# Kernel optimization log

Measured on AMD Instinct MI355X. Metric: run time of the kernel, lower is better.

The kernel has to match this reference:

```python
import jax, jax.numpy as jnp
import numpy as np

TEMPERATURE = 0.04


def _d3tod2(t):
    # 'c h w -> (h w) c'
    c, h, w = t.shape
    return jnp.transpose(t, (1, 2, 0)).reshape(h * w, c)


def setup_inputs() -> dict:
    key = jax.random.key(0)
    k1, k2 = jax.random.split(key)
    B, C, H, W = 4, 128, 96, 96
    # scale 0.05 keeps dot/temperature in a numerically sane range for exp
    x = jax.random.normal(k1, (B, C, H, W), dtype=jnp.float32) * 0.05
    label = jax.random.randint(k2, (B, 1, H, W), 0, 3, dtype=jnp.int32)
    return {"x": x, "label": label}


def reference(x, label):
    B, C, H, W = x.shape
    hw = H * W
    feat_1 = _d3tod2(x[0])                     # [HW, C]
    feat_2 = _d3tod2(x[1])                     # [HW, C]
    gt1 = label[0, 0].reshape(hw)              # [HW]
    gt2 = label[1, 0].reshape(hw)              # [HW]
    sim = jnp.exp(jnp.matmul(feat_1, feat_2.T) / TEMPERATURE)  # [HW, HW]
    mask = gt1[:, None] == gt2[None, :]        # [HW, HW] label-equality
    pos_sum = jnp.sum(jnp.where(mask, sim, jnp.zeros((), sim.dtype)))
    total_sum = jnp.sum(sim)
    loss = -jnp.log(pos_sum / total_sum) / (hw * hw)
    return loss
```

## Files before the change

### kernel.cpp

```cpp
#include <hip/hip_runtime.h>
#include <hip/hip_bf16.h>

#define HW 9216
#define CDIM 128
#define BM 256
#define BN 64
#define JT 4
#define GRID_I (HW / BM)
#define GRID_J (HW / (BN * JT))
#define NPART (GRID_I * GRID_J)
#define LDP (CDIM + 8)

using bf16 = __hip_bfloat16;
typedef __attribute__((ext_vector_type(16))) float f32x16;
typedef __attribute__((ext_vector_type(8))) short s16x8;

#define EXP_SCALE 36.067376022224085f

#if __has_builtin(__builtin_amdgcn_exp2f)
#define FEXP2(x) __builtin_amdgcn_exp2f(x)
#else
#define FEXP2(x) exp2f(x)
#endif

__global__ __launch_bounds__(256) void prep_kernel(const float* __restrict__ x,
                                                   bf16* __restrict__ feat) {
    __shared__ float tile[64][65];
    const float* xs = x + (size_t)blockIdx.z * CDIM * HW;
    bf16* fs = feat + (size_t)blockIdx.z * HW * CDIM;
    float scale = (blockIdx.z == 0) ? EXP_SCALE : 1.0f;

    int p0 = blockIdx.x * 64;
    int c0 = blockIdx.y * 64;
    int t  = threadIdx.x;

    int pc = t & 63;
    int cr = t >> 6;
#pragma unroll
    for (int i = 0; i < 16; ++i) {
        int cl = cr + i * 4;
        tile[cl][pc] = xs[(size_t)(c0 + cl) * HW + p0 + pc];
    }
    __syncthreads();

    int cc = t & 63;
    int pr = t >> 6;
#pragma unroll
    for (int i = 0; i < 16; ++i) {
        int pl = pr + i * 4;
        fs[(size_t)(p0 + pl) * CDIM + c0 + cc] = __float2bfloat16(tile[cc][pl] * scale);
    }
}

__global__ __launch_bounds__(512, 4) void simsum_kernel(const bf16* __restrict__ feat1,
                                                        const bf16* __restrict__ feat2,
                                                        const int* __restrict__ label,
                                                        float* __restrict__ partials) {
    __shared__ bf16 Bs[2][BN][LDP];
    __shared__ float red[16];

    int t    = threadIdx.x;
    int w    = t >> 6;
    int lane = t & 63;
    int cl   = lane & 31;
    int hi   = lane >> 5;

    int i0  = blockIdx.x * BM;
    int jb  = blockIdx.y * (BN * JT);
    int r0w = i0 + w * 32;

    s16x8 af[8];
    {
        const bf16* arow = &feat1[(size_t)(r0w + cl) * CDIM + hi * 8];
#pragma unroll
        for (int s = 0; s < 8; ++s)
            af[s] = *(const s16x8*)(arow + s * 16);
    }

    int4 g1i[4];
#pragma unroll
    for (int q = 0; q < 4; ++q)
        g1i[q] = *(const int4*)(&label[r0w + 4 * hi + 8 * q]);

    int srow = t >> 4;
    int sch8 = (t & 15) * 8;
    s16x8 rb[2];

    auto load_tile = [&](int tt) {
        const bf16* base = &feat2[(size_t)(jb + tt * BN + srow) * CDIM + sch8];
        rb[0] = *(const s16x8*)(base);
        rb[1] = *(const s16x8*)(base + 32 * CDIM);
    };
    auto write_tile = [&](int b) {
        *(s16x8*)(&Bs[b][srow][sch8])      = rb[0];
        *(s16x8*)(&Bs[b][srow + 32][sch8]) = rb[1];
    };

    load_tile(0);  write_tile(0);
    load_tile(1);  write_tile(1);
    load_tile(2);
    asm volatile("s_waitcnt lgkmcnt(0)" ::: "memory");
    __builtin_amdgcn_sched_barrier(0);
    __builtin_amdgcn_s_barrier();

    const int* lab2 = label + HW;
    float tot0 = 0.f, tot1 = 0.f, pos0 = 0.f, pos1 = 0.f;

#pragma unroll
    for (int tt = 0; tt < JT; ++tt) {
        int g2a = lab2[jb + tt * BN + cl];
        int g2b = lab2[jb + tt * BN + 32 + cl];

        f32x16 acc0 = {}, acc1 = {};
#pragma unroll
        for (int s = 0; s < 8; ++s) {
            const bf16* bp = &Bs[tt & 1][cl][s * 16 + hi * 8];
            s16x8 b0 = *(const s16x8*)(bp);
            s16x8 b1 = *(const s16x8*)(bp + (size_t)32 * LDP);
            acc0 = __builtin_amdgcn_mfma_f32_32x32x16_bf16(af[s], b0, acc0, 0, 0, 0);
            acc1 = __builtin_amdgcn_mfma_f32_32x32x16_bf16(af[s], b1, acc1, 0, 0, 0);
        }

        __builtin_amdgcn_sched_barrier(0);
        __builtin_amdgcn_s_barrier();

        if (tt + 2 < JT) write_tile(tt & 1);
        if (tt + 3 < JT) load_tile(tt + 3);

#pragma unroll
        for (int r = 0; r < 16; ++r) {
            int g1 = ((const int*)g1i)[r];
            float e0 = FEXP2(acc0[r]);
            tot0 += e0;
            pos0 += (g1 == g2a) ? e0 : 0.f;
            float e1 = FEXP2(acc1[r]);
            tot1 += e1;
            pos1 += (g1 == g2b) ? e1 : 0.f;
        }

        if (tt + 1 < JT) {
            asm volatile("s_waitcnt lgkmcnt(0)" ::: "memory");
            __builtin_amdgcn_sched_barrier(0);
            __builtin_amdgcn_s_barrier();
        }
    }

    float tot = tot0 + tot1, pos = pos0 + pos1;
#pragma unroll
    for (int off = 32; off; off >>= 1) {
        tot += __shfl_down(tot, off);
        pos += __shfl_down(pos, off);
    }
    if (lane == 0) { red[w * 2] = tot; red[w * 2 + 1] = pos; }
    __syncthreads();
    if (t == 0) {
        float T = 0.f, P = 0.f;
#pragma unroll
        for (int q = 0; q < 8; ++q) { T += red[q * 2]; P += red[q * 2 + 1]; }
        int bid = blockIdx.y * GRID_I + blockIdx.x;
        partials[bid * 2]     = T;
        partials[bid * 2 + 1] = P;
    }
}

__global__ __launch_bounds__(256) void finalize_kernel(const float* __restrict__ partials,
                                                       float* __restrict__ out) {
    double tot = 0.0, pos = 0.0;
    int t = threadIdx.x;
    for (int i = t; i < NPART; i += 256) {
        tot += (double)partials[i * 2];
        pos += (double)partials[i * 2 + 1];
    }
#pragma unroll
    for (int off = 32; off; off >>= 1) {
        tot += __shfl_down(tot, off);
        pos += __shfl_down(pos, off);
    }
    __shared__ double rt[4], rp[4];
    int w = t >> 6, lane = t & 63;
    if (lane == 0) { rt[w] = tot; rp[w] = pos; }
    __syncthreads();
    if (t == 0) {
        double T = rt[0] + rt[1] + rt[2] + rt[3];
        double P = rp[0] + rp[1] + rp[2] + rp[3];
        double hw2 = (double)HW * (double)HW;
        out[0] = (float)(-log(P / T) / hw2);
    }
}

extern "C" void kernel_launch(void* const* d_in, const int* in_sizes, int n_in,
                              void* d_out, int out_size, void* d_ws, size_t ws_size,
                              hipStream_t stream) {
    const float* x     = (const float*)d_in[0];
    const int*   label = (const int*)d_in[1];
    float*       out   = (float*)d_out;

    bf16*  feat  = (bf16*)d_ws;
    float* parts = (float*)((char*)d_ws + 2 * (size_t)HW * CDIM * sizeof(bf16));

    dim3 g1(HW / 64, CDIM / 64, 2);
    prep_kernel<<<g1, 256, 0, stream>>>(x, feat);

    dim3 g2(GRID_I, GRID_J);
    simsum_kernel<<<g2, 512, 0, stream>>>(feat, feat + (size_t)HW * CDIM, label, parts);

    finalize_kernel<<<1, 256, 0, stream>>>(parts, out);
}
```

Measured before the change: 50.55 us.

## Sort pixels by label so uniform tiles skip per-element mask selects

Adds a counting-sort kernel that permutes pixels of both images by label, and gathers features in that sorted order during prep. In the similarity kernel, 32x32 sub-tiles whose row and column labels are all the same reuse the tile's total exp sum for the positive sum instead of doing per-element compare-and-select. It also raises wave priority around the MFMA loop. The cost is an extra launch, a gathered and less coalesced load in prep, and a branchy path that recomputes exp for mixed-label tiles.

After: 58.40 us. 15.5% more time.

```diff
diff --git a/kernel.cpp b/kernel.cpp
--- a/kernel.cpp
+++ b/kernel.cpp
@@ -10,6 +10,7 @@
 #define GRID_J (HW / (BN * JT))
 #define NPART (GRID_I * GRID_J)
 #define LDP (CDIM + 8)
+#define SCH (HW / 512)
 
 using bf16 = __hip_bfloat16;
 typedef __attribute__((ext_vector_type(16))) float f32x16;
@@ -23,10 +24,55 @@
 #define FEXP2(x) exp2f(x)
 #endif
 
+__global__ __launch_bounds__(512) void sort_kernel(const int* __restrict__ label,
+                                                   int* __restrict__ perm,
+                                                   int* __restrict__ labs) {
+    const int side = blockIdx.x;
+    const int* L = label + side * HW;
+    int* P = perm + side * HW;
+    int* S = labs + side * HW;
+    __shared__ int cnt[3][512];
+
+    int t = threadIdx.x;
+    int l[SCH];
+    int c0 = 0, c1 = 0, c2 = 0;
+#pragma unroll
+    for (int k = 0; k < SCH; ++k) {
+        l[k] = L[t * SCH + k];
+        c0 += (l[k] == 0); c1 += (l[k] == 1); c2 += (l[k] == 2);
+    }
+    cnt[0][t] = c0; cnt[1][t] = c1; cnt[2][t] = c2;
+    __syncthreads();
+
+    for (int off = 1; off < 512; off <<= 1) {
+        int v0 = cnt[0][t], v1 = cnt[1][t], v2 = cnt[2][t];
+        int a0 = 0, a1 = 0, a2 = 0;
+        if (t >= off) { a0 = cnt[0][t - off]; a1 = cnt[1][t - off]; a2 = cnt[2][t - off]; }
+        __syncthreads();
+        cnt[0][t] = v0 + a0; cnt[1][t] = v1 + a1; cnt[2][t] = v2 + a2;
+        __syncthreads();
+    }
+
+    int i0 = cnt[0][t], i1 = cnt[1][t], i2 = cnt[2][t];
+    int tl0 = cnt[0][511], tl1 = cnt[1][511];
+    int o0 = i0 - c0;
+    int o1 = tl0 + i1 - c1;
+    int o2 = tl0 + tl1 + i2 - c2;
+#pragma unroll
+    for (int k = 0; k < SCH; ++k) {
+        int lab = l[k];
+        int pos = (lab == 0) ? o0++ : ((lab == 1) ? o1++ : o2++);
+        P[pos] = t * SCH + k;
+        S[pos] = lab;
+    }
+}
+
 __global__ __launch_bounds__(256) void prep_kernel(const float* __restrict__ x,
+                                                   const int* __restrict__ perm,
                                                    bf16* __restrict__ feat) {
     __shared__ float tile[64][65];
     const float* xs = x + (size_t)blockIdx.z * CDIM * HW;
+    const int* permS = perm + blockIdx.z * HW;
     bf16* fs = feat + (size_t)blockIdx.z * HW * CDIM;
     float scale = (blockIdx.z == 0) ? EXP_SCALE : 1.0f;
 
@@ -36,10 +82,11 @@
 
     int pc = t & 63;
     int cr = t >> 6;
+    int pidx = permS[p0 + pc];
 #pragma unroll
     for (int i = 0; i < 16; ++i) {
         int cl = cr + i * 4;
-        tile[cl][pc] = xs[(size_t)(c0 + cl) * HW + p0 + pc];
+        tile[cl][pc] = xs[(size_t)(c0 + cl) * HW + pidx];
     }
     __syncthreads();
 
@@ -54,10 +101,13 @@
 
 __global__ __launch_bounds__(512, 4) void simsum_kernel(const bf16* __restrict__ feat1,
                                                         const bf16* __restrict__ feat2,
-                                                        const int* __restrict__ label,
+                                                        const int* __restrict__ labs,
                                                         float* __restrict__ partials) {
     __shared__ bf16 Bs[2][BN][LDP];
     __shared__ float red[16];
+
+    const int* lab1s = labs;
+    const int* lab2s = labs + HW;
 
     int t    = threadIdx.x;
     int w    = t >> 6;
@@ -77,10 +127,13 @@
             af[s] = *(const s16x8*)(arow + s * 16);
     }
 
+    int rlab  = lab1s[r0w];
+    bool rowU = (rlab == lab1s[r0w + 31]);
+
     int4 g1i[4];
 #pragma unroll
     for (int q = 0; q < 4; ++q)
-        g1i[q] = *(const int4*)(&label[r0w + 4 * hi + 8 * q]);
+        g1i[q] = *(const int4*)(&lab1s[r0w + 4 * hi + 8 * q]);
 
     int srow = t >> 4;
     int sch8 = (t & 15) * 8;
@@ -103,15 +156,20 @@
     __builtin_amdgcn_sched_barrier(0);
     __builtin_amdgcn_s_barrier();
 
-    const int* lab2 = label + HW;
     float tot0 = 0.f, tot1 = 0.f, pos0 = 0.f, pos1 = 0.f;
 
 #pragma unroll
     for (int tt = 0; tt < JT; ++tt) {
-        int g2a = lab2[jb + tt * BN + cl];
-        int g2b = lab2[jb + tt * BN + 32 + cl];
+        int cb = jb + tt * BN;
+        int laA = lab2s[cb];
+        int laB = lab2s[cb + 32];
+        bool uniA = rowU && (laA == lab2s[cb + 31]);
+        bool uniB = rowU && (laB == lab2s[cb + 63]);
+        int g2a = lab2s[cb + cl];
+        int g2b = lab2s[cb + 32 + cl];
 
         f32x16 acc0 = {}, acc1 = {};
+        __builtin_amdgcn_s_setprio(1);
 #pragma unroll
         for (int s = 0; s < 8; ++s) {
             const bf16* bp = &Bs[tt & 1][cl][s * 16 + hi * 8];
@@ -120,6 +178,7 @@
             acc0 = __builtin_amdgcn_mfma_f32_32x32x16_bf16(af[s], b0, acc0, 0, 0, 0);
             acc1 = __builtin_amdgcn_mfma_f32_32x32x16_bf16(af[s], b1, acc1, 0, 0, 0);
         }
+        __builtin_amdgcn_s_setprio(0);
 
         __builtin_amdgcn_sched_barrier(0);
         __builtin_amdgcn_s_barrier();
@@ -127,15 +186,42 @@
         if (tt + 2 < JT) write_tile(tt & 1);
         if (tt + 3 < JT) load_tile(tt + 3);
 
-#pragma unroll
-        for (int r = 0; r < 16; ++r) {
-            int g1 = ((const int*)g1i)[r];
-            float e0 = FEXP2(acc0[r]);
-            tot0 += e0;
-            pos0 += (g1 == g2a) ? e0 : 0.f;
-            float e1 = FEXP2(acc1[r]);
-            tot1 += e1;
-            pos1 += (g1 == g2b) ? e1 : 0.f;
+        {
+            float a0 = 0.f, a1 = 0.f, a2 = 0.f, a3 = 0.f;
+            float b0 = 0.f, b1 = 0.f, b2 = 0.f, b3 = 0.f;
+#pragma unroll
+            for (int r = 0; r < 4; ++r) {
+                a0 += FEXP2(acc0[r]);
+                a1 += FEXP2(acc0[r + 4]);
+                a2 += FEXP2(acc0[r + 8]);
+                a3 += FEXP2(acc0[r + 12]);
+                b0 += FEXP2(acc1[r]);
+                b1 += FEXP2(acc1[r + 4]);
+                b2 += FEXP2(acc1[r + 8]);
+                b3 += FEXP2(acc1[r + 12]);
+            }
+            float csA = (a0 + a1) + (a2 + a3);
+            float csB = (b0 + b1) + (b2 + b3);
+            tot0 += csA;
+            tot1 += csB;
+            if (uniA) {
+                pos0 += (rlab == laA) ? csA : 0.f;
+            } else {
+#pragma unroll
+                for (int r = 0; r < 16; ++r) {
+                    int g1 = ((const int*)g1i)[r];
+                    pos0 += (g1 == g2a) ? FEXP2(acc0[r]) : 0.f;
+                }
+            }
+            if (uniB) {
+                pos1 += (rlab == laB) ? csB : 0.f;
+            } else {
+#pragma unroll
+                for (int r = 0; r < 16; ++r) {
+                    int g1 = ((const int*)g1i)[r];
+                    pos1 += (g1 == g2b) ? FEXP2(acc1[r]) : 0.f;
+                }
+            }
         }
 
         if (tt + 1 < JT) {
@@ -195,14 +281,19 @@
     const int*   label = (const int*)d_in[1];
     float*       out   = (float*)d_out;
 
-    bf16*  feat  = (bf16*)d_ws;
-    float* parts = (float*)((char*)d_ws + 2 * (size_t)HW * CDIM * sizeof(bf16));
+    bf16* feat = (bf16*)d_ws;
+    char* pp   = (char*)d_ws + 2 * (size_t)HW * CDIM * sizeof(bf16);
+    int*  perm = (int*)pp;
+    int*  labs = (int*)(pp + 2 * (size_t)HW * sizeof(int));
+    float* parts = (float*)(pp + 4 * (size_t)HW * sizeof(int));
+
+    sort_kernel<<<2, 512, 0, stream>>>(label, perm, labs);
 
     dim3 g1(HW / 64, CDIM / 64, 2);
-    prep_kernel<<<g1, 256, 0, stream>>>(x, feat);
+    prep_kernel<<<g1, 256, 0, stream>>>(x, perm, feat);
 
     dim3 g2(GRID_I, GRID_J);
-    simsum_kernel<<<g2, 512, 0, stream>>>(feat, feat + (size_t)HW * CDIM, label, parts);
+    simsum_kernel<<<g2, 512, 0, stream>>>(feat, feat + (size_t)HW * CDIM, labs, parts);
 
     finalize_kernel<<<1, 256, 0, stream>>>(parts, out);
 }
```
